# Optimization experiments

Hardware: AMD Instinct MI355X
Metric: run time of the kernel (lower is better)

Reference implementation:

```python
import jax, jax.numpy as jnp
import numpy as np

N_WIRES = 4
N_LAYERS = 2
PATCHES = 196  # 14x14 grid of 2x2 patches


def _bexp(a, nd):
    # broadcast angle to rank nd by appending singleton axes
    a = jnp.asarray(a)
    return a.reshape(a.shape + (1,) * (nd - a.ndim))


def _apply_ry(state, wire, angle):
    # state: [B, P, 2,2,2,2]; angle broadcastable to [B, P] or scalar
    st = jnp.moveaxis(state, 2 + wire, -1)
    c = _bexp(jnp.cos(angle * 0.5), st.ndim - 1)
    s = _bexp(jnp.sin(angle * 0.5), st.ndim - 1)
    s0, s1 = st[..., 0], st[..., 1]
    out = jnp.stack([c * s0 - s * s1, s * s0 + c * s1], axis=-1)
    return jnp.moveaxis(out, -1, 2 + wire)


def _apply_cnot(state, control, target):
    st = jnp.moveaxis(state, (2 + control, 2 + target), (-2, -1))
    st = jnp.stack([st[..., 0, :], st[..., 1, ::-1]], axis=-2)
    return jnp.moveaxis(st, (-2, -1), (2 + control, 2 + target))


def _measure_z(state):
    # PauliZ expectation on each wire: sum probs * (+1/-1)
    p = state * state  # real state => |amp|^2
    outs = []
    for w in range(N_WIRES):
        axes = tuple(a for a in range(2, 2 + N_WIRES) if a != 2 + w)
        m = p.sum(axis=axes)  # [B, P, 2]
        outs.append(m[..., 0] - m[..., 1])
    return jnp.stack(outs, axis=-1)  # [B, P, 4]


def _quanv(x, theta):
    B = x.shape[0]
    # extract 2x2 patches: order (r,c),(r,c+1),(r+1,c),(r+1,c+1)
    img = x.reshape(B, 14, 2, 14, 2).transpose(0, 1, 3, 2, 4).reshape(B, PATCHES, 4)
    state = jnp.zeros((B, PATCHES, 16), x.dtype).at[:, :, 0].set(1.0)
    state = state.reshape(B, PATCHES, 2, 2, 2, 2)
    # encoder: RY(x_i) on wire i
    for w in range(N_WIRES):
        state = _apply_ry(state, w, img[:, :, w])
    # variational layers: trainable RY per wire + CNOT ring
    for l in range(N_LAYERS):
        for w in range(N_WIRES):
            state = _apply_ry(state, w, theta[l, w])
        for w in range(N_WIRES):
            state = _apply_cnot(state, w, (w + 1) % N_WIRES)
    return _measure_z(state).reshape(B, PATCHES * N_WIRES)  # [B, 784]


def setup_inputs() -> dict:
    key = jax.random.key(0)
    k = jax.random.split(key, 6)
    B = 4096
    return {
        "x": jax.random.uniform(k[0], (B, 784), jnp.float32),
        "theta": jax.random.normal(k[1], (N_LAYERS, N_WIRES), jnp.float32),
        "W1": jax.random.normal(k[2], (784, 128), jnp.float32) * 0.05,
        "b1": jnp.zeros((128,), jnp.float32),
        "W2": jax.random.normal(k[3], (128, 10), jnp.float32) * 0.05,
        "b2": jnp.zeros((10,), jnp.float32),
    }


def reference(x, theta, W1, b1, W2, b2):
    feats = _quanv(x, theta)                 # [B, 784]
    h = jax.nn.relu(feats @ W1 + b1)          # [B, 128]
    logits = h @ W2 + b2                      # [B, 10]
    return jax.nn.log_softmax(logits, axis=-1)
```

## Files before the change

### kernel.cpp

```cpp
#include <hip/hip_runtime.h>
#include <math.h>

#define PATCHES 196
#define KPAD 800
#define MROWS 8
#define CIRC (MROWS * PATCHES)
#define THREADS 512
#define FRAG_ELEMS (25 * 64 * 8)

typedef short short8 __attribute__((ext_vector_type(8)));
typedef float f32x4 __attribute__((ext_vector_type(4)));

__device__ __forceinline__ unsigned short f2bf(float f) {
  union { float f; unsigned u; } x; x.f = f;
  unsigned r = x.u + 0x7fff + ((x.u >> 16) & 1);
  return (unsigned short)(r >> 16);
}

__global__ __launch_bounds__(256) void w1t_pack_kernel(
    const float* __restrict__ W1, unsigned short* __restrict__ w1p) {
  int idx = blockIdx.x * 256 + threadIdx.x;
  if (idx >= 128 * KPAD) return;
  int n = idx / KPAD;
  int k = idx - n * KPAD;
  float v = (k < 784) ? W1[k * 128 + n] : 0.f;
  int ki = k >> 5;
  int quad = (k & 31) >> 3;
  int j = k & 7;
  w1p[(n >> 4) * FRAG_ELEMS + (ki * 64 + quad * 16 + (n & 15)) * 8 + j] = f2bf(v);
}

__device__ __forceinline__ void apply_ry(float st[16], int bit, float c, float s) {
#pragma unroll
  for (int i = 0; i < 16; ++i) {
    if (!(i & bit)) {
      int j = i | bit;
      float a0 = st[i], a1 = st[j];
      st[i] = c * a0 - s * a1;
      st[j] = s * a0 + c * a1;
    }
  }
}

__device__ __forceinline__ void apply_cnot(float st[16], int cb, int tb) {
#pragma unroll
  for (int i = 0; i < 16; ++i) {
    if ((i & cb) && !(i & tb)) {
      int j = i | tb;
      float t = st[i]; st[i] = st[j]; st[j] = t;
    }
  }
}

__global__ __launch_bounds__(THREADS) void fused_kernel(
    const float* __restrict__ x, const float* __restrict__ theta,
    const unsigned short* __restrict__ w1p, const float* __restrict__ b1,
    const float* __restrict__ W2, const float* __restrict__ b2,
    float* __restrict__ out) {
  __shared__ unsigned short afr[FRAG_ELEMS];
  __shared__ float tc[8], ts[8];
  __shared__ float ws2[1280];
  __shared__ float hs[MROWS * 132];
  __shared__ float ls[MROWS * 10];

  const int tid = threadIdx.x;
  const int row0 = blockIdx.x * MROWS;

  {
    ushort4 z; z.x = z.y = z.z = z.w = 0;
    for (int s = tid; s < FRAG_ELEMS / 4; s += THREADS)
      reinterpret_cast<ushort4*>(afr)[s] = z;
  }
  if (tid < 8) {
    float a = 0.5f * theta[tid];
    tc[tid] = __cosf(a);
    ts[tid] = __sinf(a);
  }
  if (tid < 320)
    reinterpret_cast<float4*>(ws2)[tid] = reinterpret_cast<const float4*>(W2)[tid];

  const int nit = (tid + 3 * THREADS < CIRC) ? 4 : 3;
  float2 xa[4], xb2[4];
#pragma unroll
  for (int i = 0; i < 4; ++i) {
    if (i < nit) {
      int c = tid + i * THREADS;
      int bl = c / PATCHES;
      int p = c - bl * PATCHES;
      int pr = p / 14;
      int pc = p - pr * 14;
      const float* xb = x + (size_t)(row0 + bl) * 784 + pr * 56 + pc * 2;
      xa[i]  = *reinterpret_cast<const float2*>(xb);
      xb2[i] = *reinterpret_cast<const float2*>(xb + 28);
    }
  }
  __syncthreads();

#pragma unroll
  for (int i = 0; i < 4; ++i) {
    if (i >= nit) break;
    int c = tid + i * THREADS;
    int bl = c / PATCHES;
    int p = c - bl * PATCHES;
    float v0 = xa[i].x, v1 = xa[i].y, v2 = xb2[i].x, v3 = xb2[i].y;

    float st[16];
#pragma unroll
    for (int q = 0; q < 16; ++q) st[q] = 0.f;
    st[0] = 1.f;

    apply_ry(st, 8, __cosf(0.5f * v0), __sinf(0.5f * v0));
    apply_ry(st, 4, __cosf(0.5f * v1), __sinf(0.5f * v1));
    apply_ry(st, 2, __cosf(0.5f * v2), __sinf(0.5f * v2));
    apply_ry(st, 1, __cosf(0.5f * v3), __sinf(0.5f * v3));

#pragma unroll
    for (int l = 0; l < 2; ++l) {
      apply_ry(st, 8, tc[l * 4 + 0], ts[l * 4 + 0]);
      apply_ry(st, 4, tc[l * 4 + 1], ts[l * 4 + 1]);
      apply_ry(st, 2, tc[l * 4 + 2], ts[l * 4 + 2]);
      apply_ry(st, 1, tc[l * 4 + 3], ts[l * 4 + 3]);
      apply_cnot(st, 8, 4);
      apply_cnot(st, 4, 2);
      apply_cnot(st, 2, 1);
      apply_cnot(st, 1, 8);
    }

    float m0 = 0.f, m1 = 0.f, m2 = 0.f, m3 = 0.f;
#pragma unroll
    for (int q = 0; q < 16; ++q) {
      float p2 = st[q] * st[q];
      m0 += (q & 8) ? -p2 : p2;
      m1 += (q & 4) ? -p2 : p2;
      m2 += (q & 2) ? -p2 : p2;
      m3 += (q & 1) ? -p2 : p2;
    }

    int K = p * 4;
    int ki = K >> 5;
    int quad = (K & 31) >> 3;
    int j0 = K & 7;
    ushort4 o;
    o.x = f2bf(m0); o.y = f2bf(m1); o.z = f2bf(m2); o.w = f2bf(m3);
    *reinterpret_cast<ushort4*>(afr + (ki * 64 + quad * 16 + bl) * 8 + j0) = o;
  }
  __syncthreads();

  const int lane = tid & 63;
  const int wave = tid >> 6;
  const int m = lane & 15;
  const int quad = lane >> 4;

  {
    const unsigned short* bp = w1p + (size_t)wave * FRAG_ELEMS + lane * 8;
    const unsigned short* apl = afr + lane * 8;

    f32x4 acc = {0.f, 0.f, 0.f, 0.f};

#pragma unroll
    for (int kc = 0; kc < 5; ++kc) {
      short8 a[5], b[5];
#pragma unroll
      for (int u = 0; u < 5; ++u) {
        const int ki = kc * 5 + u;
        a[u] = *reinterpret_cast<const short8*>(apl + ki * 512);
        b[u] = *reinterpret_cast<const short8*>(bp + ki * 512);
      }
#pragma unroll
      for (int u = 0; u < 5; ++u)
        acc = __builtin_amdgcn_mfma_f32_16x16x32_bf16(a[u], b[u], acc, 0, 0, 0);
    }

    if (quad < 2) {
      const int col = wave * 16 + m;
      const float bc = b1[col];
#pragma unroll
      for (int r = 0; r < 4; ++r)
        hs[(quad * 4 + r) * 132 + col] = fmaxf(acc[r] + bc, 0.f);
    }
  }
  __syncthreads();

  if (tid < MROWS * 10) {
    const int r = tid / 10;
    const int k = tid - r * 10;
    float a = b2[k];
    const float* hr = hs + r * 132;
#pragma unroll 8
    for (int jj = 0; jj < 128; ++jj) a = fmaf(hr[jj], ws2[jj * 10 + k], a);
    ls[tid] = a;
  }
  __syncthreads();

  if (tid < MROWS) {
    const int r = tid;
    float mx = ls[r * 10];
#pragma unroll
    for (int k = 1; k < 10; ++k) mx = fmaxf(mx, ls[r * 10 + k]);
    float sum = 0.f;
#pragma unroll
    for (int k = 0; k < 10; ++k) sum += __expf(ls[r * 10 + k] - mx);
    const float lse = mx + __logf(sum);
    float* orow = out + (size_t)(row0 + r) * 10;
#pragma unroll
    for (int k = 0; k < 10; ++k) orow[k] = ls[r * 10 + k] - lse;
  }
}

extern "C" void kernel_launch(void* const* d_in, const int* in_sizes, int n_in,
                              void* d_out, int out_size, void* d_ws, size_t ws_size,
                              hipStream_t stream) {
  const float* x     = (const float*)d_in[0];
  const float* theta = (const float*)d_in[1];
  const float* W1    = (const float*)d_in[2];
  const float* b1    = (const float*)d_in[3];
  const float* W2    = (const float*)d_in[4];
  const float* b2    = (const float*)d_in[5];
  float* out = (float*)d_out;

  const int B = in_sizes[0] / 784;

  unsigned short* w1p = (unsigned short*)d_ws;

  w1t_pack_kernel<<<(128 * KPAD + 255) / 256, 256, 0, stream>>>(W1, w1p);
  fused_kernel<<<B / MROWS, THREADS, 0, stream>>>(x, theta, w1p, b1, W2, b2, out);
}
```

Baseline: 86.00 us.

## Compute encoder state as product state and software-pipeline patch loads

The four encoder RY rotations on |0000> are replaced by a closed-form tensor product of cos/sin terms, which removes most of the encoder arithmetic. Theta cos/sin moves from shared memory into per-thread registers computed redundantly. The circuit loop becomes a non-unrolled loop that prefetches the next patch's pixels, and the MFMA k-loop is no longer unrolled. Together these aim to cut register pressure and instruction count, at the cost of less latency hiding from unrolling.

```diff
diff --git a/kernel.cpp b/kernel.cpp
--- a/kernel.cpp
+++ b/kernel.cpp
@@ -58,7 +58,6 @@
     const float* __restrict__ W2, const float* __restrict__ b2,
     float* __restrict__ out) {
   __shared__ unsigned short afr[FRAG_ELEMS];
-  __shared__ float tc[8], ts[8];
   __shared__ float ws2[1280];
   __shared__ float hs[MROWS * 132];
   __shared__ float ls[MROWS * 10];
@@ -71,48 +70,55 @@
     for (int s = tid; s < FRAG_ELEMS / 4; s += THREADS)
       reinterpret_cast<ushort4*>(afr)[s] = z;
   }
-  if (tid < 8) {
-    float a = 0.5f * theta[tid];
-    tc[tid] = __cosf(a);
-    ts[tid] = __sinf(a);
-  }
   if (tid < 320)
     reinterpret_cast<float4*>(ws2)[tid] = reinterpret_cast<const float4*>(W2)[tid];
 
-  const int nit = (tid + 3 * THREADS < CIRC) ? 4 : 3;
-  float2 xa[4], xb2[4];
-#pragma unroll
-  for (int i = 0; i < 4; ++i) {
-    if (i < nit) {
-      int c = tid + i * THREADS;
-      int bl = c / PATCHES;
-      int p = c - bl * PATCHES;
-      int pr = p / 14;
-      int pc = p - pr * 14;
-      const float* xb = x + (size_t)(row0 + bl) * 784 + pr * 56 + pc * 2;
-      xa[i]  = *reinterpret_cast<const float2*>(xb);
-      xb2[i] = *reinterpret_cast<const float2*>(xb + 28);
-    }
-  }
-  __syncthreads();
-
-#pragma unroll
-  for (int i = 0; i < 4; ++i) {
-    if (i >= nit) break;
-    int c = tid + i * THREADS;
-    int bl = c / PATCHES;
-    int p = c - bl * PATCHES;
-    float v0 = xa[i].x, v1 = xa[i].y, v2 = xb2[i].x, v3 = xb2[i].y;
+  float tc[8], ts[8];
+#pragma unroll
+  for (int w = 0; w < 8; ++w) {
+    float a = 0.5f * theta[w];
+    tc[w] = __cosf(a);
+    ts[w] = __sinf(a);
+  }
+
+  const int nit = (CIRC - tid + THREADS - 1) / THREADS;
+  float2 xcA, xcB;
+  {
+    int bl = tid / PATCHES;
+    int p = tid - bl * PATCHES;
+    int pr = p / 14, pc = p - pr * 14;
+    const float* xp = x + (size_t)(row0 + bl) * 784 + pr * 56 + pc * 2;
+    xcA = *reinterpret_cast<const float2*>(xp);
+    xcB = *reinterpret_cast<const float2*>(xp + 28);
+  }
+  __syncthreads();
+
+#pragma unroll 1
+  for (int i = 0; i < nit; ++i) {
+    const int c = tid + i * THREADS;
+    float2 xnA = xcA, xnB = xcB;
+    if (i + 1 < nit) {
+      const int cn = c + THREADS;
+      int bl = cn / PATCHES;
+      int p = cn - bl * PATCHES;
+      int pr = p / 14, pc = p - pr * 14;
+      const float* xp = x + (size_t)(row0 + bl) * 784 + pr * 56 + pc * 2;
+      xnA = *reinterpret_cast<const float2*>(xp);
+      xnB = *reinterpret_cast<const float2*>(xp + 28);
+    }
+
+    float c0 = __cosf(0.5f * xcA.x), s0 = __sinf(0.5f * xcA.x);
+    float c1 = __cosf(0.5f * xcA.y), s1 = __sinf(0.5f * xcA.y);
+    float c2 = __cosf(0.5f * xcB.x), s2 = __sinf(0.5f * xcB.x);
+    float c3 = __cosf(0.5f * xcB.y), s3 = __sinf(0.5f * xcB.y);
+    float u00 = c0 * c1, u01 = c0 * s1, u10 = s0 * c1, u11 = s0 * s1;
+    float w00 = c2 * c3, w01 = c2 * s3, w10 = s2 * c3, w11 = s2 * s3;
 
     float st[16];
-#pragma unroll
-    for (int q = 0; q < 16; ++q) st[q] = 0.f;
-    st[0] = 1.f;
-
-    apply_ry(st, 8, __cosf(0.5f * v0), __sinf(0.5f * v0));
-    apply_ry(st, 4, __cosf(0.5f * v1), __sinf(0.5f * v1));
-    apply_ry(st, 2, __cosf(0.5f * v2), __sinf(0.5f * v2));
-    apply_ry(st, 1, __cosf(0.5f * v3), __sinf(0.5f * v3));
+    st[ 0] = u00 * w00; st[ 1] = u00 * w01; st[ 2] = u00 * w10; st[ 3] = u00 * w11;
+    st[ 4] = u01 * w00; st[ 5] = u01 * w01; st[ 6] = u01 * w10; st[ 7] = u01 * w11;
+    st[ 8] = u10 * w00; st[ 9] = u10 * w01; st[10] = u10 * w10; st[11] = u10 * w11;
+    st[12] = u11 * w00; st[13] = u11 * w01; st[14] = u11 * w10; st[15] = u11 * w11;
 
 #pragma unroll
     for (int l = 0; l < 2; ++l) {
@@ -136,13 +142,19 @@
       m3 += (q & 1) ? -p2 : p2;
     }
 
-    int K = p * 4;
-    int ki = K >> 5;
-    int quad = (K & 31) >> 3;
-    int j0 = K & 7;
-    ushort4 o;
-    o.x = f2bf(m0); o.y = f2bf(m1); o.z = f2bf(m2); o.w = f2bf(m3);
-    *reinterpret_cast<ushort4*>(afr + (ki * 64 + quad * 16 + bl) * 8 + j0) = o;
+    {
+      int bl = c / PATCHES;
+      int p = c - bl * PATCHES;
+      int K = p * 4;
+      int ki = K >> 5;
+      int quad = (K & 31) >> 3;
+      int j0 = K & 7;
+      ushort4 o;
+      o.x = f2bf(m0); o.y = f2bf(m1); o.z = f2bf(m2); o.w = f2bf(m3);
+      *reinterpret_cast<ushort4*>(afr + (ki * 64 + quad * 16 + bl) * 8 + j0) = o;
+    }
+
+    xcA = xnA; xcB = xnB;
   }
   __syncthreads();
 
@@ -157,7 +169,7 @@
 
     f32x4 acc = {0.f, 0.f, 0.f, 0.f};
 
-#pragma unroll
+#pragma unroll 1
     for (int kc = 0; kc < 5; ++kc) {
       short8 a[5], b[5];
 #pragma unroll
```

Result: faster. 83.98 us (-2.3%).
